# Performance work log

Measured on AMD Instinct MI355X. Metric: run time of the kernel, lower is better.

The kernel has to match this reference:

```python
import jax, jax.numpy as jnp
import numpy as np

B, CQ, CC, COUT, H, W = 32, 256, 3, 256, 32, 32
INTER = CQ // 2
HC, WC = 224, 224
EPS = 1e-5


def setup_inputs() -> dict:
    key = jax.random.key(0)
    ks = jax.random.split(key, 12)
    s = lambda fan_in: 1.0 / np.sqrt(fan_in)
    return {
        "query_feat": jax.random.normal(ks[0], (B, CQ, H, W), jnp.float32),
        "context_feat": jax.random.normal(ks[1], (B, CC, HC, WC), jnp.float32),
        "Wq": jax.random.uniform(ks[2], (INTER, CQ), jnp.float32, -s(CQ), s(CQ)),
        "bq": jax.random.uniform(ks[3], (INTER,), jnp.float32, -s(CQ), s(CQ)),
        "Wk": jax.random.uniform(ks[4], (INTER, CC), jnp.float32, -s(CC), s(CC)),
        "bk": jax.random.uniform(ks[5], (INTER,), jnp.float32, -s(CC), s(CC)),
        "Wv": jax.random.uniform(ks[6], (CQ, CC), jnp.float32, -s(CC), s(CC)),
        "bv": jax.random.uniform(ks[7], (CQ,), jnp.float32, -s(CC), s(CC)),
        "Wp": jax.random.uniform(ks[8], (COUT, CQ), jnp.float32, -s(CQ), s(CQ)),
        "bp": jax.random.uniform(ks[9], (COUT,), jnp.float32, -s(CQ), s(CQ)),
        "gamma": jnp.ones((COUT,), jnp.float32),
        "beta": jnp.zeros((COUT,), jnp.float32),
    }


def _conv1x1(x, Wmat, b):
    # x: [B,Cin,H,W], Wmat: [Cout,Cin] -> [B,Cout,H,W]
    return jnp.einsum("oc,bchw->bohw", Wmat, x) + b[None, :, None, None]


def reference(query_feat, context_feat, Wq, bq, Wk, bk, Wv, bv, Wp, bp, gamma, beta):
    Bn, Cq, Hn, Wn = query_feat.shape
    HWn = Hn * Wn
    # bilinear resize, align_corners=False, no antialias (matches F.interpolate)
    ctx = jax.image.resize(context_feat, (Bn, context_feat.shape[1], Hn, Wn),
                           method="linear", antialias=False)
    q = _conv1x1(query_feat, Wq, bq).reshape(Bn, -1, HWn)   # [B,inter,HW]
    k = _conv1x1(ctx, Wk, bk).reshape(Bn, -1, HWn)          # [B,inter,HW]
    v = _conv1x1(ctx, Wv, bv).reshape(Bn, Cq, HWn)          # [B,Cq,HW]
    scores = jnp.einsum("bci,bcj->bij", q, k)               # [B,HW,HW]
    probs = jax.nn.softmax(scores, axis=-1)
    # attended_v[b,c,i] = sum_j v[b,c,j] * probs[b,i,j]
    attended = jnp.einsum("bcj,bij->bci", v, probs).reshape(Bn, Cq, Hn, Wn)
    fused = _conv1x1(query_feat + attended, Wp, bp)         # [B,Cout,H,W]
    # GroupNorm with 1 group: normalize over (C,H,W) per sample
    mu = jnp.mean(fused, axis=(1, 2, 3), keepdims=True)
    var = jnp.var(fused, axis=(1, 2, 3), keepdims=True)
    normed = (fused - mu) * jax.lax.rsqrt(var + EPS)
    return normed * gamma[None, :, None, None] + beta[None, :, None, None]
```

## Files before the change

### kernel.cpp

```cpp
#include <hip/hip_runtime.h>
#include <hip/hip_bf16.h>

#define WS_M4    0
#define WS_M0    1024
#define WS_G4    1056
#define WS_BSUM  2080
#define WS_BSSQ  2112
#define WS_WPB   2144
#define WS_CP    34912
#define WS_CTX   165984

typedef __attribute__((ext_vector_type(8))) short short8;
typedef __attribute__((ext_vector_type(4))) float floatx4;

__device__ inline unsigned short f2bf(float x) {
    unsigned u = __float_as_uint(x);
    return (unsigned short)((u + 0x7FFFu + ((u >> 16) & 1u)) >> 16);
}

__global__ __launch_bounds__(256) void sca_pre(
    const float* __restrict__ Wq, const float* __restrict__ bq,
    const float* __restrict__ Wk, const float* __restrict__ bk,
    const float* __restrict__ Wv, const float* __restrict__ bv,
    const float* __restrict__ Wp, const float* __restrict__ bp,
    const float* __restrict__ ctxin, float* __restrict__ ws)
{
    int tid = threadIdx.x;
    int blk = blockIdx.x;
    if (blk < 4) {
        __shared__ float WkL[384];
        __shared__ float bqL[128];
        __shared__ float redM[4][64][3];
        int o0 = blk << 6;
        if (tid < 128) bqL[tid] = bq[tid];
        for (int idx = tid; idx < 384; idx += 256) WkL[idx] = Wk[idx];
        __syncthreads();
        int o64 = tid & 63, cg = tid >> 6;
        float m0v = 0.f, m1v = 0.f, m2v = 0.f;
        for (int c0 = cg * 32; c0 < cg * 32 + 32; c0 += 16) {
            float q[16];
#pragma unroll
            for (int j = 0; j < 16; ++j) q[j] = Wq[(c0 + j) * 256 + o0 + o64];
#pragma unroll
            for (int j = 0; j < 16; ++j) {
                int c = c0 + j;
                m0v = fmaf(WkL[c * 3 + 0], q[j], m0v);
                m1v = fmaf(WkL[c * 3 + 1], q[j], m1v);
                m2v = fmaf(WkL[c * 3 + 2], q[j], m2v);
            }
        }
        redM[cg][o64][0] = m0v; redM[cg][o64][1] = m1v; redM[cg][o64][2] = m2v;
        __syncthreads();
        if (tid < 64) {
            float r0 = redM[0][tid][0] + redM[1][tid][0] + redM[2][tid][0] + redM[3][tid][0];
            float r1 = redM[0][tid][1] + redM[1][tid][1] + redM[2][tid][1] + redM[3][tid][1];
            float r2 = redM[0][tid][2] + redM[1][tid][2] + redM[2][tid][2] + redM[3][tid][2];
            ((float4*)(ws + WS_M4))[o0 + tid] = make_float4(r0, r1, r2, 0.f);
        }
        if (blk == 0) {
            if (tid < 3) {
                float s = 0.f;
                for (int c = 0; c < 128; ++c) s = fmaf(WkL[c * 3 + tid], bqL[c], s);
                ws[WS_M0 + tid] = s;
            }
            if (tid < 64) ws[WS_BSUM + tid] = 0.f;
        }
    } else if (blk < 36) {
        __shared__ float WvL[768];
        __shared__ float bvL[256];
        for (int idx = tid; idx < 768; idx += 256) WvL[idx] = Wv[idx];
        bvL[tid] = bv[tid];
        __syncthreads();
        int idx = (blk - 4) * 2048 + tid * 8;
        int o = idx >> 8;
        int kt = (tid & 31) >> 2, quad = tid & 3;
        const float4* s = (const float4*)(Wp + idx);
        float4 x0 = s[0], x1 = s[1];
        uint4 v;
        v.x = (unsigned)f2bf(x0.x) | ((unsigned)f2bf(x0.y) << 16);
        v.y = (unsigned)f2bf(x0.z) | ((unsigned)f2bf(x0.w) << 16);
        v.z = (unsigned)f2bf(x1.x) | ((unsigned)f2bf(x1.y) << 16);
        v.w = (unsigned)f2bf(x1.z) | ((unsigned)f2bf(x1.w) << 16);
        int slot = (((o >> 4) * 8 + kt) * 64) + quad * 16 + (o & 15);
        ((uint4*)((unsigned short*)(ws + WS_WPB)))[slot] = v;
        int c0 = idx & 255;
        float xv[8] = {x0.x, x0.y, x0.z, x0.w, x1.x, x1.y, x1.z, x1.w};
        float g0 = 0.f, g1 = 0.f, g2 = 0.f, gb = 0.f;
#pragma unroll
        for (int j = 0; j < 8; ++j) {
            int c = c0 + j;
            g0 = fmaf(xv[j], WvL[c * 3 + 0], g0);
            g1 = fmaf(xv[j], WvL[c * 3 + 1], g1);
            g2 = fmaf(xv[j], WvL[c * 3 + 2], g2);
            gb = fmaf(xv[j], bvL[c], gb);
        }
#pragma unroll
        for (int off = 1; off < 32; off <<= 1) {
            g0 += __shfl_xor(g0, off);
            g1 += __shfl_xor(g1, off);
            g2 += __shfl_xor(g2, off);
            gb += __shfl_xor(gb, off);
        }
        if ((tid & 31) == 0)
            ((float4*)(ws + WS_G4))[o] = make_float4(g0, g1, g2, gb + bp[o]);
    } else {
        int g = (blk - 36) * 256 + tid;
        int b = g >> 10, j = g & 1023;
        int y = j >> 5, x = j & 31;
        const float* src = ctxin + (size_t)b * 150528;
        int p = (7 * y + 3) * 224 + (7 * x + 3);
        ((float4*)(ws + WS_CTX))[g] =
            make_float4(src[p], src[p + 50176], src[p + 100352], 0.f);
    }
}

__global__ __launch_bounds__(256, 4) void sca_attn(const float* __restrict__ Q,
                                                   float* __restrict__ ws)
{
    __shared__ float cs0[1024];
    __shared__ float cs1[1024];
    __shared__ float cs2[1024];
    __shared__ float red[4][8][12];
    __shared__ float4 av4[32];

    int tid = threadIdx.x;
    int blk = blockIdx.x;
    int b  = blk >> 5;
    int i0 = (blk & 31) << 5;
    int lane = tid & 63, w = tid >> 6;
    int iq = tid & 7, kg = tid >> 3;

    {
        const float4* cg4 = ((const float4*)(ws + WS_CTX)) + ((size_t)b << 10);
#pragma unroll
        for (int s4 = 0; s4 < 4; ++s4) {
            int j = s4 * 256 + tid;
            float4 v = cg4[j];
            cs0[j] = v.x; cs1[j] = v.y; cs2[j] = v.z;
        }
    }

    const float4* M4 = (const float4*)(ws + WS_M4);
    const float* Qp = Q + ((size_t)b << 18) + ((size_t)(kg * 8) << 10) + i0 + iq * 4;
    float a00=0.f,a01=0.f,a02=0.f,a03=0.f;
    float a10=0.f,a11=0.f,a12=0.f,a13=0.f;
    float a20=0.f,a21=0.f,a22=0.f,a23=0.f;
#pragma unroll
    for (int s = 0; s < 8; ++s) {
        float4 qv = *(const float4*)(Qp + ((size_t)s << 10));
        float4 mv = M4[kg * 8 + s];
        a00 = fmaf(mv.x, qv.x, a00); a01 = fmaf(mv.x, qv.y, a01); a02 = fmaf(mv.x, qv.z, a02); a03 = fmaf(mv.x, qv.w, a03);
        a10 = fmaf(mv.y, qv.x, a10); a11 = fmaf(mv.y, qv.y, a11); a12 = fmaf(mv.y, qv.z, a12); a13 = fmaf(mv.y, qv.w, a13);
        a20 = fmaf(mv.z, qv.x, a20); a21 = fmaf(mv.z, qv.y, a21); a22 = fmaf(mv.z, qv.z, a22); a23 = fmaf(mv.z, qv.w, a23);
    }
    a00 += __shfl_xor(a00,8); a00 += __shfl_xor(a00,16); a00 += __shfl_xor(a00,32);
    a01 += __shfl_xor(a01,8); a01 += __shfl_xor(a01,16); a01 += __shfl_xor(a01,32);
    a02 += __shfl_xor(a02,8); a02 += __shfl_xor(a02,16); a02 += __shfl_xor(a02,32);
    a03 += __shfl_xor(a03,8); a03 += __shfl_xor(a03,16); a03 += __shfl_xor(a03,32);
    a10 += __shfl_xor(a10,8); a10 += __shfl_xor(a10,16); a10 += __shfl_xor(a10,32);
    a11 += __shfl_xor(a11,8); a11 += __shfl_xor(a11,16); a11 += __shfl_xor(a11,32);
    a12 += __shfl_xor(a12,8); a12 += __shfl_xor(a12,16); a12 += __shfl_xor(a12,32);
    a13 += __shfl_xor(a13,8); a13 += __shfl_xor(a13,16); a13 += __shfl_xor(a13,32);
    a20 += __shfl_xor(a20,8); a20 += __shfl_xor(a20,16); a20 += __shfl_xor(a20,32);
    a21 += __shfl_xor(a21,8); a21 += __shfl_xor(a21,16); a21 += __shfl_xor(a21,32);
    a22 += __shfl_xor(a22,8); a22 += __shfl_xor(a22,16); a22 += __shfl_xor(a22,32);
    a23 += __shfl_xor(a23,8); a23 += __shfl_xor(a23,16); a23 += __shfl_xor(a23,32);
    if (lane < 8) {
        red[w][lane][0]=a00; red[w][lane][1]=a01; red[w][lane][2] =a02; red[w][lane][3] =a03;
        red[w][lane][4]=a10; red[w][lane][5]=a11; red[w][lane][6] =a12; red[w][lane][7] =a13;
        red[w][lane][8]=a20; red[w][lane][9]=a21; red[w][lane][10]=a22; red[w][lane][11]=a23;
    }
    __syncthreads();
    if (tid < 32) {
        int iqq = tid >> 2, e = tid & 3;
        float r0 = red[0][iqq][0+e] + red[1][iqq][0+e] + red[2][iqq][0+e] + red[3][iqq][0+e] + ws[WS_M0 + 0];
        float r1 = red[0][iqq][4+e] + red[1][iqq][4+e] + red[2][iqq][4+e] + red[3][iqq][4+e] + ws[WS_M0 + 1];
        float r2 = red[0][iqq][8+e] + red[1][iqq][8+e] + red[2][iqq][8+e] + red[3][iqq][8+e] + ws[WS_M0 + 2];
        av4[tid] = make_float4(r0, r1, r2, 0.f);
    }
    __syncthreads();

    {
        int qi = tid >> 3, sl = tid & 7;
        float4 a = av4[qi];
        float sh = 6.0f * (fabsf(a.x) + fabsf(a.y) + fabsf(a.z));
        float d = 0.f, s0 = 0.f, s1 = 0.f, s2 = 0.f;
#pragma unroll 4
        for (int jj = 0; jj < 128; ++jj) {
            int j = (jj << 3) + sl;
            float c0 = cs0[j], c1 = cs1[j], c2 = cs2[j];
            float sc = fmaf(a.x, c0, fmaf(a.y, c1, a.z * c2));
            float e = __expf(sc - sh);
            d += e;
            s0 = fmaf(e, c0, s0);
            s1 = fmaf(e, c1, s1);
            s2 = fmaf(e, c2, s2);
        }
        d  += __shfl_xor(d, 1);  d  += __shfl_xor(d, 2);  d  += __shfl_xor(d, 4);
        s0 += __shfl_xor(s0, 1); s0 += __shfl_xor(s0, 2); s0 += __shfl_xor(s0, 4);
        s1 += __shfl_xor(s1, 1); s1 += __shfl_xor(s1, 2); s1 += __shfl_xor(s1, 4);
        s2 += __shfl_xor(s2, 1); s2 += __shfl_xor(s2, 2); s2 += __shfl_xor(s2, 4);
        if (sl == 0) {
            float inv = 1.0f / d;
            ((float4*)(ws + WS_CP))[(b << 10) + i0 + qi] =
                make_float4(s0 * inv, s1 * inv, s2 * inv, 0.f);
        }
    }
}

__global__ __launch_bounds__(512, 2) void sca_gemm(const float* __restrict__ Q,
                                                   float* __restrict__ ws,
                                                   float* __restrict__ out)
{
    __shared__ uint4 QL[2048];
    __shared__ float sred[16];

    int tid = threadIdx.x;
    int blk = blockIdx.x;
    int b  = blk >> 3;
    int oh = (blk >> 2) & 1;
    int i0 = (blk & 3) << 8;
    int lane = tid & 63, w = tid >> 6;
    int m = lane & 15, quad = lane >> 4;

    const short8* Apack = (const short8*)((const unsigned short*)(ws + WS_WPB));
    int otile = oh * 8 + w;

    floatx4 acc[16] = {};
    const float* Qbase = Q + ((size_t)b << 18) + i0 + (lane << 2);

    for (int c = 0; c < 4; ++c) {
        float4 qv[8];
#pragma unroll
        for (int s = 0; s < 8; ++s)
            qv[s] = *(const float4*)(Qbase + ((size_t)(c * 64 + w * 8 + s) << 10));
        __syncthreads();
#pragma unroll
        for (int e = 0; e < 4; ++e) {
            const float* q0 = (const float*)&qv[0];
            uint4 v;
            v.x = (unsigned)f2bf(((const float*)&qv[0])[e]) | ((unsigned)f2bf(((const float*)&qv[1])[e]) << 16);
            v.y = (unsigned)f2bf(((const float*)&qv[2])[e]) | ((unsigned)f2bf(((const float*)&qv[3])[e]) << 16);
            v.z = (unsigned)f2bf(((const float*)&qv[4])[e]) | ((unsigned)f2bf(((const float*)&qv[5])[e]) << 16);
            v.w = (unsigned)f2bf(((const float*)&qv[6])[e]) | ((unsigned)f2bf(((const float*)&qv[7])[e]) << 16);
            int i = (lane << 2) + e;
            int gs = w ^ (i & 7) ^ ((i >> 2) & 7);
            QL[i * 8 + gs] = v;
            (void)q0;
        }
        __syncthreads();
#pragma unroll
        for (int kk = 0; kk < 2; ++kk) {
            short8 af = Apack[((otile * 8) + (c * 2 + kk)) * 64 + lane];
#pragma unroll
            for (int it = 0; it < 16; ++it) {
                int i = it * 16 + m;
                int g = kk * 4 + quad;
                int gs = g ^ (i & 7) ^ ((i >> 2) & 7);
                short8 bf = ((const short8*)QL)[i * 8 + gs];
                acc[it] = __builtin_amdgcn_mfma_f32_16x16x32_bf16(
                    af, bf, acc[it], 0, 0, 0);
            }
        }
    }

    const floatx4* G4 = (const floatx4*)(ws + WS_G4);
    const float4* CP4 = ((const float4*)(ws + WS_CP)) + ((size_t)b << 10) + i0;
    floatx4 gv[4];
#pragma unroll
    for (int r = 0; r < 4; ++r) gv[r] = G4[oh * 128 + w * 16 + quad * 4 + r];
    float lsum = 0.f, lssq = 0.f;
#pragma unroll
    for (int it = 0; it < 16; ++it) {
        float4 cp = CP4[it * 16 + m];
#pragma unroll
        for (int r = 0; r < 4; ++r) {
            int o = oh * 128 + w * 16 + quad * 4 + r;
            float v = acc[it][r]
                    + gv[r][0] * cp.x + gv[r][1] * cp.y + gv[r][2] * cp.z + gv[r][3];
            out[(((size_t)(b * 256 + o)) << 10) + i0 + it * 16 + m] = v;
            lsum += v; lssq = fmaf(v, v, lssq);
        }
    }
#pragma unroll
    for (int off = 32; off > 0; off >>= 1) {
        lsum += __shfl_down(lsum, off);
        lssq += __shfl_down(lssq, off);
    }
    if (lane == 0) { sred[w] = lsum; sred[8 + w] = lssq; }
    __syncthreads();
    if (tid == 0) {
        float s = 0.f, q2 = 0.f;
#pragma unroll
        for (int j = 0; j < 8; ++j) { s += sred[j]; q2 += sred[8 + j]; }
        atomicAdd(ws + WS_BSUM + b, s);
        atomicAdd(ws + WS_BSSQ + b, q2);
    }
}

__global__ __launch_bounds__(256) void sca_norm(float* __restrict__ out,
                                                const float* __restrict__ ws,
                                                const float* __restrict__ gamma,
                                                const float* __restrict__ beta)
{
    const float inv_n = 1.0f / 262144.0f;
#pragma unroll
    for (int r = 0; r < 4; ++r) {
        size_t idx = (size_t)r * 524288 + (size_t)blockIdx.x * 256 + threadIdx.x;
        float4 v = ((const float4*)out)[idx];
        size_t base = idx << 2;
        int b = (int)(base >> 18);
        int o = (int)((base >> 10) & 255);
        float mean = ws[WS_BSUM + b] * inv_n;
        float var  = fmaf(ws[WS_BSSQ + b], inv_n, -mean * mean);
        float rs = rsqrtf(var + 1e-5f);
        float ga = gamma[o] * rs;
        float be = fmaf(-mean, ga, beta[o]);
        v.x = fmaf(v.x, ga, be);
        v.y = fmaf(v.y, ga, be);
        v.z = fmaf(v.z, ga, be);
        v.w = fmaf(v.w, ga, be);
        ((float4*)out)[idx] = v;
    }
}

extern "C" void kernel_launch(void* const* d_in, const int* in_sizes, int n_in,
                              void* d_out, int out_size, void* d_ws, size_t ws_size,
                              hipStream_t stream)
{
    const float* Q     = (const float*)d_in[0];
    const float* ctxf  = (const float*)d_in[1];
    const float* Wq    = (const float*)d_in[2];
    const float* bq    = (const float*)d_in[3];
    const float* Wk    = (const float*)d_in[4];
    const float* bk    = (const float*)d_in[5];
    const float* Wv    = (const float*)d_in[6];
    const float* bv    = (const float*)d_in[7];
    const float* Wp    = (const float*)d_in[8];
    const float* bp    = (const float*)d_in[9];
    const float* gamma = (const float*)d_in[10];
    const float* beta  = (const float*)d_in[11];
    float* ws  = (float*)d_ws;
    float* out = (float*)d_out;

    sca_pre <<<164,  256, 0, stream>>>(Wq, bq, Wk, bk, Wv, bv, Wp, bp, ctxf, ws);
    sca_attn<<<1024, 256, 0, stream>>>(Q, ws);
    sca_gemm<<<256,  512, 0, stream>>>(Q, ws, out);
    sca_norm<<<2048, 256, 0, stream>>>(out, ws, gamma, beta);
}
```

Baseline: 160.5 us.

## Fuse attention, projection GEMM and GroupNorm into one kernel with grid barrier

Folds the attention-vector computation and the softmax-weighted context average into the projection GEMM kernel, reusing the Q tiles already loaded, so the separate attention kernel and its workspace round trip go away. GroupNorm is applied in registers after a software grid-wide barrier (an atomic counter with spin-wait) that waits for all per-sample sum and sum-of-squares atomics, which removes the separate norm kernel and the second pass over the output. This relies on all 256 blocks being co-resident, and the barrier counter is zeroed only in the pre kernel. Shared memory use rises considerably, which may lower occupancy.

Result: slower. 165.1 us (+2.9%).

```diff
diff --git a/kernel.cpp b/kernel.cpp
--- a/kernel.cpp
+++ b/kernel.cpp
@@ -6,9 +6,9 @@
 #define WS_G4    1056
 #define WS_BSUM  2080
 #define WS_BSSQ  2112
-#define WS_WPB   2144
-#define WS_CP    34912
-#define WS_CTX   165984
+#define WS_BAR   2144
+#define WS_WPB   2176
+#define WS_CTX   34944
 
 typedef __attribute__((ext_vector_type(8))) short short8;
 typedef __attribute__((ext_vector_type(4))) float floatx4;
@@ -63,7 +63,7 @@
                 for (int c = 0; c < 128; ++c) s = fmaf(WkL[c * 3 + tid], bqL[c], s);
                 ws[WS_M0 + tid] = s;
             }
-            if (tid < 64) ws[WS_BSUM + tid] = 0.f;
+            if (tid < 65) ws[WS_BSUM + tid] = 0.f;
         }
     } else if (blk < 36) {
         __shared__ float WvL[768];
@@ -114,106 +114,19 @@
     }
 }
 
-__global__ __launch_bounds__(256, 4) void sca_attn(const float* __restrict__ Q,
-                                                   float* __restrict__ ws)
-{
-    __shared__ float cs0[1024];
-    __shared__ float cs1[1024];
-    __shared__ float cs2[1024];
-    __shared__ float red[4][8][12];
-    __shared__ float4 av4[32];
-
-    int tid = threadIdx.x;
-    int blk = blockIdx.x;
-    int b  = blk >> 5;
-    int i0 = (blk & 31) << 5;
-    int lane = tid & 63, w = tid >> 6;
-    int iq = tid & 7, kg = tid >> 3;
-
-    {
-        const float4* cg4 = ((const float4*)(ws + WS_CTX)) + ((size_t)b << 10);
-#pragma unroll
-        for (int s4 = 0; s4 < 4; ++s4) {
-            int j = s4 * 256 + tid;
-            float4 v = cg4[j];
-            cs0[j] = v.x; cs1[j] = v.y; cs2[j] = v.z;
-        }
-    }
-
-    const float4* M4 = (const float4*)(ws + WS_M4);
-    const float* Qp = Q + ((size_t)b << 18) + ((size_t)(kg * 8) << 10) + i0 + iq * 4;
-    float a00=0.f,a01=0.f,a02=0.f,a03=0.f;
-    float a10=0.f,a11=0.f,a12=0.f,a13=0.f;
-    float a20=0.f,a21=0.f,a22=0.f,a23=0.f;
-#pragma unroll
-    for (int s = 0; s < 8; ++s) {
-        float4 qv = *(const float4*)(Qp + ((size_t)s << 10));
-        float4 mv = M4[kg * 8 + s];
-        a00 = fmaf(mv.x, qv.x, a00); a01 = fmaf(mv.x, qv.y, a01); a02 = fmaf(mv.x, qv.z, a02); a03 = fmaf(mv.x, qv.w, a03);
-        a10 = fmaf(mv.y, qv.x, a10); a11 = fmaf(mv.y, qv.y, a11); a12 = fmaf(mv.y, qv.z, a12); a13 = fmaf(mv.y, qv.w, a13);
-        a20 = fmaf(mv.z, qv.x, a20); a21 = fmaf(mv.z, qv.y, a21); a22 = fmaf(mv.z, qv.z, a22); a23 = fmaf(mv.z, qv.w, a23);
-    }
-    a00 += __shfl_xor(a00,8); a00 += __shfl_xor(a00,16); a00 += __shfl_xor(a00,32);
-    a01 += __shfl_xor(a01,8); a01 += __shfl_xor(a01,16); a01 += __shfl_xor(a01,32);
-    a02 += __shfl_xor(a02,8); a02 += __shfl_xor(a02,16); a02 += __shfl_xor(a02,32);
-    a03 += __shfl_xor(a03,8); a03 += __shfl_xor(a03,16); a03 += __shfl_xor(a03,32);
-    a10 += __shfl_xor(a10,8); a10 += __shfl_xor(a10,16); a10 += __shfl_xor(a10,32);
-    a11 += __shfl_xor(a11,8); a11 += __shfl_xor(a11,16); a11 += __shfl_xor(a11,32);
-    a12 += __shfl_xor(a12,8); a12 += __shfl_xor(a12,16); a12 += __shfl_xor(a12,32);
-    a13 += __shfl_xor(a13,8); a13 += __shfl_xor(a13,16); a13 += __shfl_xor(a13,32);
-    a20 += __shfl_xor(a20,8); a20 += __shfl_xor(a20,16); a20 += __shfl_xor(a20,32);
-    a21 += __shfl_xor(a21,8); a21 += __shfl_xor(a21,16); a21 += __shfl_xor(a21,32);
-    a22 += __shfl_xor(a22,8); a22 += __shfl_xor(a22,16); a22 += __shfl_xor(a22,32);
-    a23 += __shfl_xor(a23,8); a23 += __shfl_xor(a23,16); a23 += __shfl_xor(a23,32);
-    if (lane < 8) {
-        red[w][lane][0]=a00; red[w][lane][1]=a01; red[w][lane][2] =a02; red[w][lane][3] =a03;
-        red[w][lane][4]=a10; red[w][lane][5]=a11; red[w][lane][6] =a12; red[w][lane][7] =a13;
-        red[w][lane][8]=a20; red[w][lane][9]=a21; red[w][lane][10]=a22; red[w][lane][11]=a23;
-    }
-    __syncthreads();
-    if (tid < 32) {
-        int iqq = tid >> 2, e = tid & 3;
-        float r0 = red[0][iqq][0+e] + red[1][iqq][0+e] + red[2][iqq][0+e] + red[3][iqq][0+e] + ws[WS_M0 + 0];
-        float r1 = red[0][iqq][4+e] + red[1][iqq][4+e] + red[2][iqq][4+e] + red[3][iqq][4+e] + ws[WS_M0 + 1];
-        float r2 = red[0][iqq][8+e] + red[1][iqq][8+e] + red[2][iqq][8+e] + red[3][iqq][8+e] + ws[WS_M0 + 2];
-        av4[tid] = make_float4(r0, r1, r2, 0.f);
-    }
-    __syncthreads();
-
-    {
-        int qi = tid >> 3, sl = tid & 7;
-        float4 a = av4[qi];
-        float sh = 6.0f * (fabsf(a.x) + fabsf(a.y) + fabsf(a.z));
-        float d = 0.f, s0 = 0.f, s1 = 0.f, s2 = 0.f;
-#pragma unroll 4
-        for (int jj = 0; jj < 128; ++jj) {
-            int j = (jj << 3) + sl;
-            float c0 = cs0[j], c1 = cs1[j], c2 = cs2[j];
-            float sc = fmaf(a.x, c0, fmaf(a.y, c1, a.z * c2));
-            float e = __expf(sc - sh);
-            d += e;
-            s0 = fmaf(e, c0, s0);
-            s1 = fmaf(e, c1, s1);
-            s2 = fmaf(e, c2, s2);
-        }
-        d  += __shfl_xor(d, 1);  d  += __shfl_xor(d, 2);  d  += __shfl_xor(d, 4);
-        s0 += __shfl_xor(s0, 1); s0 += __shfl_xor(s0, 2); s0 += __shfl_xor(s0, 4);
-        s1 += __shfl_xor(s1, 1); s1 += __shfl_xor(s1, 2); s1 += __shfl_xor(s1, 4);
-        s2 += __shfl_xor(s2, 1); s2 += __shfl_xor(s2, 2); s2 += __shfl_xor(s2, 4);
-        if (sl == 0) {
-            float inv = 1.0f / d;
-            ((float4*)(ws + WS_CP))[(b << 10) + i0 + qi] =
-                make_float4(s0 * inv, s1 * inv, s2 * inv, 0.f);
-        }
-    }
-}
-
-__global__ __launch_bounds__(512, 2) void sca_gemm(const float* __restrict__ Q,
+__global__ __launch_bounds__(512, 2) void sca_mega(const float* __restrict__ Q,
                                                    float* __restrict__ ws,
+                                                   const float* __restrict__ gamma,
+                                                   const float* __restrict__ beta,
                                                    float* __restrict__ out)
 {
+    __shared__ float4 cs4[1024];
+    __shared__ float4 Ms4[256];
     __shared__ uint4 QL[2048];
-    __shared__ float sred[16];
+    __shared__ float red[8][64][13];
+    __shared__ float4 av4[256];
+    __shared__ float4 cps[256];
+    __shared__ float sred[18];
 
     int tid = threadIdx.x;
     int blk = blockIdx.x;
@@ -223,10 +136,19 @@
     int lane = tid & 63, w = tid >> 6;
     int m = lane & 15, quad = lane >> 4;
 
+    {
+        const float4* cg4 = ((const float4*)(ws + WS_CTX)) + ((size_t)b << 10);
+        cs4[tid] = cg4[tid];
+        cs4[512 + tid] = cg4[512 + tid];
+        if (tid < 256) Ms4[tid] = ((const float4*)(ws + WS_M4))[tid];
+    }
+    __syncthreads();
+
     const short8* Apack = (const short8*)((const unsigned short*)(ws + WS_WPB));
     int otile = oh * 8 + w;
 
     floatx4 acc[16] = {};
+    float ap[12] = {};
     const float* Qbase = Q + ((size_t)b << 18) + i0 + (lane << 2);
 
     for (int c = 0; c < 4; ++c) {
@@ -234,10 +156,20 @@
 #pragma unroll
         for (int s = 0; s < 8; ++s)
             qv[s] = *(const float4*)(Qbase + ((size_t)(c * 64 + w * 8 + s) << 10));
-        __syncthreads();
+        if (c > 0) __syncthreads();
+#pragma unroll
+        for (int s = 0; s < 8; ++s) {
+            float4 mv = Ms4[c * 64 + w * 8 + s];
+#pragma unroll
+            for (int e = 0; e < 4; ++e) {
+                float qe = ((const float*)&qv[s])[e];
+                ap[0 + e] = fmaf(mv.x, qe, ap[0 + e]);
+                ap[4 + e] = fmaf(mv.y, qe, ap[4 + e]);
+                ap[8 + e] = fmaf(mv.z, qe, ap[8 + e]);
+            }
+        }
 #pragma unroll
         for (int e = 0; e < 4; ++e) {
-            const float* q0 = (const float*)&qv[0];
             uint4 v;
             v.x = (unsigned)f2bf(((const float*)&qv[0])[e]) | ((unsigned)f2bf(((const float*)&qv[1])[e]) << 16);
             v.y = (unsigned)f2bf(((const float*)&qv[2])[e]) | ((unsigned)f2bf(((const float*)&qv[3])[e]) << 16);
@@ -246,7 +178,6 @@
             int i = (lane << 2) + e;
             int gs = w ^ (i & 7) ^ ((i >> 2) & 7);
             QL[i * 8 + gs] = v;
-            (void)q0;
         }
         __syncthreads();
 #pragma unroll
@@ -264,21 +195,84 @@
         }
     }
 
+#pragma unroll
+    for (int c2 = 0; c2 < 12; ++c2) red[w][lane][c2] = ap[c2];
+    __syncthreads();
+    if (tid < 256) {
+        int iq = tid >> 2, e = tid & 3;
+        float r0 = ws[WS_M0 + 0], r1 = ws[WS_M0 + 1], r2 = ws[WS_M0 + 2];
+#pragma unroll
+        for (int wv = 0; wv < 8; ++wv) {
+            r0 += red[wv][iq][0 + e];
+            r1 += red[wv][iq][4 + e];
+            r2 += red[wv][iq][8 + e];
+        }
+        av4[tid] = make_float4(r0, r1, r2, 0.f);
+    }
+    __syncthreads();
+
+    {
+        int sl = tid & 7, qg = tid >> 3;
+        float4 a0 = av4[qg], a1 = av4[qg + 64], a2 = av4[qg + 128], a3 = av4[qg + 192];
+        float sh0 = 6.0f * (fabsf(a0.x) + fabsf(a0.y) + fabsf(a0.z));
+        float sh1 = 6.0f * (fabsf(a1.x) + fabsf(a1.y) + fabsf(a1.z));
+        float sh2 = 6.0f * (fabsf(a2.x) + fabsf(a2.y) + fabsf(a2.z));
+        float sh3 = 6.0f * (fabsf(a3.x) + fabsf(a3.y) + fabsf(a3.z));
+        float d0=0.f,x0=0.f,y0=0.f,z0=0.f, d1=0.f,x1=0.f,y1=0.f,z1=0.f;
+        float d2=0.f,x2=0.f,y2=0.f,z2=0.f, d3=0.f,x3=0.f,y3=0.f,z3=0.f;
+#pragma unroll 4
+        for (int jj = 0; jj < 128; ++jj) {
+            float4 cv = cs4[(jj << 3) + sl];
+            float sc, e;
+            sc = fmaf(a0.x, cv.x, fmaf(a0.y, cv.y, a0.z * cv.z));
+            e = __expf(sc - sh0);
+            d0 += e; x0 = fmaf(e, cv.x, x0); y0 = fmaf(e, cv.y, y0); z0 = fmaf(e, cv.z, z0);
+            sc = fmaf(a1.x, cv.x, fmaf(a1.y, cv.y, a1.z * cv.z));
+            e = __expf(sc - sh1);
+            d1 += e; x1 = fmaf(e, cv.x, x1); y1 = fmaf(e, cv.y, y1); z1 = fmaf(e, cv.z, z1);
+            sc = fmaf(a2.x, cv.x, fmaf(a2.y, cv.y, a2.z * cv.z));
+            e = __expf(sc - sh2);
+            d2 += e; x2 = fmaf(e, cv.x, x2); y2 = fmaf(e, cv.y, y2); z2 = fmaf(e, cv.z, z2);
+            sc = fmaf(a3.x, cv.x, fmaf(a3.y, cv.y, a3.z * cv.z));
+            e = __expf(sc - sh3);
+            d3 += e; x3 = fmaf(e, cv.x, x3); y3 = fmaf(e, cv.y, y3); z3 = fmaf(e, cv.z, z3);
+        }
+#pragma unroll
+        for (int off = 1; off < 8; off <<= 1) {
+            d0 += __shfl_xor(d0, off); x0 += __shfl_xor(x0, off); y0 += __shfl_xor(y0, off); z0 += __shfl_xor(z0, off);
+            d1 += __shfl_xor(d1, off); x1 += __shfl_xor(x1, off); y1 += __shfl_xor(y1, off); z1 += __shfl_xor(z1, off);
+            d2 += __shfl_xor(d2, off); x2 += __shfl_xor(x2, off); y2 += __shfl_xor(y2, off); z2 += __shfl_xor(z2, off);
+            d3 += __shfl_xor(d3, off); x3 += __shfl_xor(x3, off); y3 += __shfl_xor(y3, off); z3 += __shfl_xor(z3, off);
+        }
+        if (sl == 0) {
+            float i0v = 1.0f / d0, i1v = 1.0f / d1, i2v = 1.0f / d2, i3v = 1.0f / d3;
+            cps[qg      ] = make_float4(x0 * i0v, y0 * i0v, z0 * i0v, 0.f);
+            cps[qg +  64] = make_float4(x1 * i1v, y1 * i1v, z1 * i1v, 0.f);
+            cps[qg + 128] = make_float4(x2 * i2v, y2 * i2v, z2 * i2v, 0.f);
+            cps[qg + 192] = make_float4(x3 * i3v, y3 * i3v, z3 * i3v, 0.f);
+        }
+    }
+    __syncthreads();
+
     const floatx4* G4 = (const floatx4*)(ws + WS_G4);
-    const float4* CP4 = ((const float4*)(ws + WS_CP)) + ((size_t)b << 10) + i0;
     floatx4 gv[4];
-#pragma unroll
-    for (int r = 0; r < 4; ++r) gv[r] = G4[oh * 128 + w * 16 + quad * 4 + r];
+    float gaw[4], btw[4];
+#pragma unroll
+    for (int r = 0; r < 4; ++r) {
+        int o = oh * 128 + w * 16 + quad * 4 + r;
+        gv[r] = G4[o];
+        gaw[r] = gamma[o];
+        btw[r] = beta[o];
+    }
     float lsum = 0.f, lssq = 0.f;
 #pragma unroll
     for (int it = 0; it < 16; ++it) {
-        float4 cp = CP4[it * 16 + m];
+        float4 cp = cps[it * 16 + m];
 #pragma unroll
         for (int r = 0; r < 4; ++r) {
-            int o = oh * 128 + w * 16 + quad * 4 + r;
             float v = acc[it][r]
                     + gv[r][0] * cp.x + gv[r][1] * cp.y + gv[r][2] * cp.z + gv[r][3];
-            out[(((size_t)(b * 256 + o)) << 10) + i0 + it * 16 + m] = v;
+            acc[it][r] = v;
             lsum += v; lssq = fmaf(v, v, lssq);
         }
     }
@@ -289,38 +283,40 @@
     }
     if (lane == 0) { sred[w] = lsum; sred[8 + w] = lssq; }
     __syncthreads();
+
     if (tid == 0) {
         float s = 0.f, q2 = 0.f;
 #pragma unroll
         for (int j = 0; j < 8; ++j) { s += sred[j]; q2 += sred[8 + j]; }
         atomicAdd(ws + WS_BSUM + b, s);
         atomicAdd(ws + WS_BSSQ + b, q2);
-    }
-}
-
-__global__ __launch_bounds__(256) void sca_norm(float* __restrict__ out,
-                                                const float* __restrict__ ws,
-                                                const float* __restrict__ gamma,
-                                                const float* __restrict__ beta)
-{
+        __threadfence();
+        int* bar = (int*)(ws + WS_BAR);
+        atomicAdd(bar, 1);
+        while (atomicAdd(bar, 0) < 256) __builtin_amdgcn_s_sleep(2);
+        sred[16] = atomicAdd(ws + WS_BSUM + b, 0.0f);
+        sred[17] = atomicAdd(ws + WS_BSSQ + b, 0.0f);
+    }
+    __syncthreads();
+
     const float inv_n = 1.0f / 262144.0f;
+    float mean = sred[16] * inv_n;
+    float var  = fmaf(sred[17], inv_n, -mean * mean);
+    float rs = rsqrtf(var + 1e-5f);
+    float gm[4], gb2[4];
 #pragma unroll
     for (int r = 0; r < 4; ++r) {
-        size_t idx = (size_t)r * 524288 + (size_t)blockIdx.x * 256 + threadIdx.x;
-        float4 v = ((const float4*)out)[idx];
-        size_t base = idx << 2;
-        int b = (int)(base >> 18);
-        int o = (int)((base >> 10) & 255);
-        float mean = ws[WS_BSUM + b] * inv_n;
-        float var  = fmaf(ws[WS_BSSQ + b], inv_n, -mean * mean);
-        float rs = rsqrtf(var + 1e-5f);
-        float ga = gamma[o] * rs;
-        float be = fmaf(-mean, ga, beta[o]);
-        v.x = fmaf(v.x, ga, be);
-        v.y = fmaf(v.y, ga, be);
-        v.z = fmaf(v.z, ga, be);
-        v.w = fmaf(v.w, ga, be);
-        ((float4*)out)[idx] = v;
+        gm[r] = gaw[r] * rs;
+        gb2[r] = fmaf(-mean, gm[r], btw[r]);
+    }
+#pragma unroll
+    for (int it = 0; it < 16; ++it) {
+#pragma unroll
+        for (int r = 0; r < 4; ++r) {
+            int o = oh * 128 + w * 16 + quad * 4 + r;
+            out[(((size_t)(b * 256 + o)) << 10) + i0 + it * 16 + m] =
+                fmaf(acc[it][r], gm[r], gb2[r]);
+        }
     }
 }
 
@@ -343,8 +339,6 @@
     float* ws  = (float*)d_ws;
     float* out = (float*)d_out;
 
-    sca_pre <<<164,  256, 0, stream>>>(Wq, bq, Wk, bk, Wv, bv, Wp, bp, ctxf, ws);
-    sca_attn<<<1024, 256, 0, stream>>>(Q, ws);
-    sca_gemm<<<256,  512, 0, stream>>>(Q, ws, out);
-    sca_norm<<<2048, 256, 0, stream>>>(out, ws, gamma, beta);
+    sca_pre <<<164, 256, 0, stream>>>(Wq, bq, Wk, bk, Wv, bv, Wp, bp, ctxf, ws);
+    sca_mega<<<256, 512, 0, stream>>>(Q, ws, gamma, beta, out);
 }
```
